# Kernel optimization log

Hardware: AMD Instinct MI355X
Metric: run time of the kernel (lower is better)

Reference implementation:

```python
import jax, jax.numpy as jnp
import numpy as np

BATCH = 32
IN_SHAPE = (64, 64)
OUT_SHAPE = (128, 128)


def setup_inputs() -> dict:
    key = jax.random.key(0)
    k1, k2 = jax.random.split(key)
    y = jax.random.normal(k1, (BATCH, *IN_SHAPE), dtype=jnp.float32)
    # normalized sample coordinates in [0,1), one per input dim
    xnew = jax.random.uniform(k2, (BATCH, *OUT_SHAPE, len(IN_SHAPE)), dtype=jnp.float32)
    return {"y": y, "xnew": xnew}


def reference(y, xnew):
    # y: [B, S1, S2]; xnew: [B, H, W, 2] with coords in [0,1)
    B = y.shape[0]
    s1, s2 = IN_SHAPE
    P = int(np.prod(OUT_SHAPE))
    x = xnew.reshape(B, P, 2)  # [B, P, 2]

    # FFT over spatial dims (dims 1..), as in torch.fft.fftn(..., dim=(1,2))
    F = jnp.fft.fftn(y, axes=(1, 2))  # [B, S1, S2] complex64

    # signed integer frequencies per dim (trigonometric interpolation)
    f1 = jnp.fft.fftfreq(s1).astype(jnp.float32) * s1  # [S1]
    f2 = jnp.fft.fftfreq(s2).astype(jnp.float32) * s2  # [S2]

    two_pi_i = 2j * jnp.pi
    # per-dim complex phase factors; separable NUFFT-type-2 evaluation
    E1 = jnp.exp(two_pi_i * x[..., 0:1] * f1)  # [B, P, S1]
    E2 = jnp.exp(two_pi_i * x[..., 1:2] * f2)  # [B, P, S2]

    # ynew[b,p] = (1/(S1*S2)) * sum_{k,m} F[b,k,m] E1[b,p,k] E2[b,p,m]
    ynew = jnp.einsum('bkm,bpk,bpm->bp', F, E1, E2) / (s1 * s2)
    ynew = jnp.real(ynew)
    return ynew.reshape(B, *OUT_SHAPE)
```

## Files before the change

kernel.cpp:

```cpp
#include <hip/hip_runtime.h>
#include <math.h>

#define PI_F  3.14159265358979323846f
#define C64_F 0.99879545620517239271f
#define S64_F 0.04906767432741801426f

typedef _Float16 f16x8 __attribute__((ext_vector_type(8)));
typedef float    f32x4 __attribute__((ext_vector_type(4)));

__device__ __forceinline__ float sinpi_hw(float x) { return __builtin_amdgcn_sinf(0.5f * x); }
__device__ __forceinline__ float cospi_hw(float x) { return __builtin_amdgcn_cosf(0.5f * x); }


__global__ __launch_bounds__(256, 3)
void fourier_interp_mfma(const float* __restrict__ y,
                         const float* __restrict__ xnew,
                         float* __restrict__ out)
{
    __shared__ __align__(16) _Float16 Yth[64 * 72];
    __shared__ __align__(16) _Float16 Ytl[64 * 72];
    __shared__ float2 tab[64];
    __shared__ float4 S1[256];
    __shared__ float4 S2[256];
    __shared__ int    NS1[256], NS2[256];
    __shared__ float  Wpart[4];

    const int tid    = threadIdx.x;
    const int batch  = blockIdx.x >> 6;
    const int seg    = blockIdx.x & 63;
    const int gpbase = (batch << 14) + (seg << 8);

    float wsum = 0.0f;
    {
        const float4* srcY = (const float4*)(y + (batch << 12));
#pragma unroll
        for (int i = 0; i < 4; ++i) {
            const int f = tid + (i << 8);
            const float4 v = srcY[f];
            const int k = f >> 4;
            const int n = (f & 15) << 2;
            _Float16 h;
            h = (_Float16)v.x; Yth[(n+0)*72 + k] = h; Ytl[(n+0)*72 + k] = (_Float16)(v.x - (float)h);
            h = (_Float16)v.y; Yth[(n+1)*72 + k] = h; Ytl[(n+1)*72 + k] = (_Float16)(v.y - (float)h);
            h = (_Float16)v.z; Yth[(n+2)*72 + k] = h; Ytl[(n+2)*72 + k] = (_Float16)(v.z - (float)h);
            h = (_Float16)v.w; Yth[(n+3)*72 + k] = h; Ytl[(n+3)*72 + k] = (_Float16)(v.w - (float)h);
            const float sv = (v.x - v.y) + (v.z - v.w);
            wsum += (k & 1) ? -sv : sv;
        }
    }
#pragma unroll
    for (int off = 32; off > 0; off >>= 1)
        wsum += __shfl_down(wsum, off, 64);
    if ((tid & 63) == 0) Wpart[tid >> 6] = wsum;

    {
        const float2 xv = ((const float2*)xnew)[gpbase + tid];
        {
            const float x = xv.x;
            const float sx = sinpi_hw(x), cx = cospi_hw(x);
            const float g = x * 64.0f;
            const float j = rintf(g);
            const float fr = g - j;
            const int  ji = (int)j;
            const float sf = sinpi_hw(fr);
            const float s64 = (ji & 1) ? -sf : sf;
            const float d = x - j * 0.015625f;
            const float cf = (fr == 0.0f) ? 64.0f
                : sf * cospi_hw(d) * __builtin_amdgcn_rcpf(sinpi_hw(d));
            S1[tid]  = make_float4(sx, cx, s64, cf);
            NS1[tid] = ji & 63;
        }
        {
            const float x = xv.y;
            const float sx = sinpi_hw(x), cx = cospi_hw(x);
            const float g = x * 64.0f;
            const float j = rintf(g);
            const float fr = g - j;
            const int  ji = (int)j;
            const float sf = sinpi_hw(fr);
            const float s64 = (ji & 1) ? -sf : sf;
            const float d = x - j * 0.015625f;
            const float cf = (fr == 0.0f) ? 64.0f
                : sf * cospi_hw(d) * __builtin_amdgcn_rcpf(sinpi_hw(d));
            S2[tid]  = make_float4(sx, cx, s64, cf);
            NS2[tid] = ji & 63;
        }
    }
    if (tid < 64)
        tab[tid] = make_float2(cospi_hw((float)tid * (1.0f / 64.0f)),
                               sinpi_hw((float)tid * (1.0f / 64.0f)));
    __syncthreads();

    const float W = (Wpart[0] + Wpart[1]) + (Wpart[2] + Wpart[3]);

    const int lane = tid & 63;
    const int wv   = tid >> 6;
    const int quad = lane >> 4;
    const int lrow = lane & 15;

    f16x8 Ah[4][2], Al[4][2];
#pragma unroll
    for (int nt = 0; nt < 4; ++nt)
#pragma unroll
        for (int kt = 0; kt < 2; ++kt) {
            const int off = ((nt << 4) + lrow) * 72 + (kt << 5) + (quad << 3);
            Ah[nt][kt] = *(const f16x8*)&Yth[off];
            Al[nt][kt] = *(const f16x8*)&Ytl[off];
        }

#pragma unroll 1
    for (int mt = 0; mt < 4; ++mt) {
        const int mtbase = (wv << 6) + (mt << 4);
        const float4 s1 = S1[mtbase + lrow];
        const int n1fix = NS1[mtbase + lrow];

        f32x4 acc[4];
#pragma unroll
        for (int nt = 0; nt < 4; ++nt) acc[nt] = (f32x4){0.f, 0.f, 0.f, 0.f};

#pragma unroll
        for (int kt = 0; kt < 2; ++kt) {
            const int n1b = (kt << 5) + (quad << 3);
            const float2 t0 = tab[n1b];
            float st = s1.x * t0.x - s1.y * t0.y;
            float ct = s1.y * t0.x + s1.x * t0.y;
            f16x8 bh, bl;
#pragma unroll
            for (int j = 0; j < 8; ++j) {
                const float sgn = (j & 1) ? -s1.z : s1.z;
                float c = sgn * ct * __builtin_amdgcn_rcpf(st);
                c = (n1b + j == n1fix) ? s1.w : c;
                const _Float16 h = (_Float16)c;
                bh[j] = h;
                bl[j] = (_Float16)(c - (float)h);
                if (j < 7) {
                    const float st2 = st * C64_F - ct * S64_F;
                    ct = ct * C64_F + st * S64_F;
                    st = st2;
                }
            }
#pragma unroll
            for (int nt = 0; nt < 4; ++nt) {
                acc[nt] = __builtin_amdgcn_mfma_f32_16x16x32_f16(Ah[nt][kt], bh, acc[nt], 0, 0, 0);
                acc[nt] = __builtin_amdgcn_mfma_f32_16x16x32_f16(Ah[nt][kt], bl, acc[nt], 0, 0, 0);
                acc[nt] = __builtin_amdgcn_mfma_f32_16x16x32_f16(Al[nt][kt], bh, acc[nt], 0, 0, 0);
            }
        }

        const float4 s2 = S2[mtbase + lrow];
        const int n2fix = NS2[mtbase + lrow];
        float red = 0.0f;
#pragma unroll
        for (int nt = 0; nt < 4; ++nt) {
            const int n2b = (nt << 4) + (quad << 2);
            const float2 tb = tab[n2b];
            float st = s2.x * tb.x - s2.y * tb.y;
            float ct = s2.y * tb.x + s2.x * tb.y;
#pragma unroll
            for (int reg = 0; reg < 4; ++reg) {
                const float sgn = (reg & 1) ? -s2.z : s2.z;
                float c = sgn * ct * __builtin_amdgcn_rcpf(st);
                c = (n2b + reg == n2fix) ? s2.w : c;
                red = fmaf(c, acc[nt][reg], red);
                if (reg < 3) {
                    const float st2 = st * C64_F - ct * S64_F;
                    ct = ct * C64_F + st * S64_F;
                    st = st2;
                }
            }
        }
        red += __shfl_xor(red, 16, 64);
        red += __shfl_xor(red, 32, 64);
        if (lane < 16) {
            const float r = red - s1.z * s2.z * W;
            out[gpbase + mtbase + lane] = r * (1.0f / 4096.0f);
        }
    }
}

extern "C" void kernel_launch(void* const* d_in, const int* in_sizes, int n_in,
                              void* d_out, int out_size, void* d_ws, size_t ws_size,
                              hipStream_t stream)
{
    const float* y    = (const float*)d_in[0];
    const float* xnew = (const float*)d_in[1];
    float* out        = (float*)d_out;

    fourier_interp_mfma<<<2048, 256, 0, stream>>>(y, xnew, out);
}
```

Baseline: 86.97 us.

## Drop fp16 split-precision MFMA terms and process 512 points per block

Removes the hi/lo fp16 error-compensation scheme, so each tile now issues one MFMA per k-step instead of three, and the low-part shared array and registers are gone. It also doubles the points handled per block (512 instead of 256) and halves the grid, which amortises the per-block Y staging and transpose over more output points. The cost is accuracy: both the Cotangent-kernel weights and the input values are now rounded to plain fp16, which could exceed the tolerance. Fewer blocks also means less parallelism across the GPU.

```diff
diff --git a/kernel.cpp b/kernel.cpp
--- a/kernel.cpp
+++ b/kernel.cpp
@@ -18,17 +18,16 @@
                          float* __restrict__ out)
 {
     __shared__ __align__(16) _Float16 Yth[64 * 72];
-    __shared__ __align__(16) _Float16 Ytl[64 * 72];
     __shared__ float2 tab[64];
-    __shared__ float4 S1[256];
-    __shared__ float4 S2[256];
-    __shared__ int    NS1[256], NS2[256];
+    __shared__ float4 S1[512];
+    __shared__ float4 S2[512];
+    __shared__ int    NS1[512], NS2[512];
     __shared__ float  Wpart[4];
 
     const int tid    = threadIdx.x;
-    const int batch  = blockIdx.x >> 6;
-    const int seg    = blockIdx.x & 63;
-    const int gpbase = (batch << 14) + (seg << 8);
+    const int batch  = blockIdx.x >> 5;
+    const int seg    = blockIdx.x & 31;
+    const int gpbase = (batch << 14) + (seg << 9);
 
     float wsum = 0.0f;
     {
@@ -39,11 +38,10 @@
             const float4 v = srcY[f];
             const int k = f >> 4;
             const int n = (f & 15) << 2;
-            _Float16 h;
-            h = (_Float16)v.x; Yth[(n+0)*72 + k] = h; Ytl[(n+0)*72 + k] = (_Float16)(v.x - (float)h);
-            h = (_Float16)v.y; Yth[(n+1)*72 + k] = h; Ytl[(n+1)*72 + k] = (_Float16)(v.y - (float)h);
-            h = (_Float16)v.z; Yth[(n+2)*72 + k] = h; Ytl[(n+2)*72 + k] = (_Float16)(v.z - (float)h);
-            h = (_Float16)v.w; Yth[(n+3)*72 + k] = h; Ytl[(n+3)*72 + k] = (_Float16)(v.w - (float)h);
+            Yth[(n+0)*72 + k] = (_Float16)v.x;
+            Yth[(n+1)*72 + k] = (_Float16)v.y;
+            Yth[(n+2)*72 + k] = (_Float16)v.z;
+            Yth[(n+3)*72 + k] = (_Float16)v.w;
             const float sv = (v.x - v.y) + (v.z - v.w);
             wsum += (k & 1) ? -sv : sv;
         }
@@ -53,8 +51,10 @@
         wsum += __shfl_down(wsum, off, 64);
     if ((tid & 63) == 0) Wpart[tid >> 6] = wsum;
 
-    {
-        const float2 xv = ((const float2*)xnew)[gpbase + tid];
+#pragma unroll
+    for (int sp = 0; sp < 2; ++sp) {
+        const int idx = tid + (sp << 8);
+        const float2 xv = ((const float2*)xnew)[gpbase + idx];
         {
             const float x = xv.x;
             const float sx = sinpi_hw(x), cx = cospi_hw(x);
@@ -67,8 +67,8 @@
             const float d = x - j * 0.015625f;
             const float cf = (fr == 0.0f) ? 64.0f
                 : sf * cospi_hw(d) * __builtin_amdgcn_rcpf(sinpi_hw(d));
-            S1[tid]  = make_float4(sx, cx, s64, cf);
-            NS1[tid] = ji & 63;
+            S1[idx]  = make_float4(sx, cx, s64, cf);
+            NS1[idx] = ji & 63;
         }
         {
             const float x = xv.y;
@@ -82,8 +82,8 @@
             const float d = x - j * 0.015625f;
             const float cf = (fr == 0.0f) ? 64.0f
                 : sf * cospi_hw(d) * __builtin_amdgcn_rcpf(sinpi_hw(d));
-            S2[tid]  = make_float4(sx, cx, s64, cf);
-            NS2[tid] = ji & 63;
+            S2[idx]  = make_float4(sx, cx, s64, cf);
+            NS2[idx] = ji & 63;
         }
     }
     if (tid < 64)
@@ -98,19 +98,18 @@
     const int quad = lane >> 4;
     const int lrow = lane & 15;
 
-    f16x8 Ah[4][2], Al[4][2];
+    f16x8 Ah[4][2];
 #pragma unroll
     for (int nt = 0; nt < 4; ++nt)
 #pragma unroll
         for (int kt = 0; kt < 2; ++kt) {
             const int off = ((nt << 4) + lrow) * 72 + (kt << 5) + (quad << 3);
             Ah[nt][kt] = *(const f16x8*)&Yth[off];
-            Al[nt][kt] = *(const f16x8*)&Ytl[off];
         }
 
 #pragma unroll 1
-    for (int mt = 0; mt < 4; ++mt) {
-        const int mtbase = (wv << 6) + (mt << 4);
+    for (int mt = 0; mt < 8; ++mt) {
+        const int mtbase = (wv << 7) + (mt << 4);
         const float4 s1 = S1[mtbase + lrow];
         const int n1fix = NS1[mtbase + lrow];
 
@@ -124,15 +123,13 @@
             const float2 t0 = tab[n1b];
             float st = s1.x * t0.x - s1.y * t0.y;
             float ct = s1.y * t0.x + s1.x * t0.y;
-            f16x8 bh, bl;
+            f16x8 bh;
 #pragma unroll
             for (int j = 0; j < 8; ++j) {
                 const float sgn = (j & 1) ? -s1.z : s1.z;
                 float c = sgn * ct * __builtin_amdgcn_rcpf(st);
                 c = (n1b + j == n1fix) ? s1.w : c;
-                const _Float16 h = (_Float16)c;
-                bh[j] = h;
-                bl[j] = (_Float16)(c - (float)h);
+                bh[j] = (_Float16)c;
                 if (j < 7) {
                     const float st2 = st * C64_F - ct * S64_F;
                     ct = ct * C64_F + st * S64_F;
@@ -140,11 +137,8 @@
                 }
             }
 #pragma unroll
-            for (int nt = 0; nt < 4; ++nt) {
+            for (int nt = 0; nt < 4; ++nt)
                 acc[nt] = __builtin_amdgcn_mfma_f32_16x16x32_f16(Ah[nt][kt], bh, acc[nt], 0, 0, 0);
-                acc[nt] = __builtin_amdgcn_mfma_f32_16x16x32_f16(Ah[nt][kt], bl, acc[nt], 0, 0, 0);
-                acc[nt] = __builtin_amdgcn_mfma_f32_16x16x32_f16(Al[nt][kt], bh, acc[nt], 0, 0, 0);
-            }
         }
 
         const float4 s2 = S2[mtbase + lrow];
@@ -186,5 +180,5 @@
     const float* xnew = (const float*)d_in[1];
     float* out        = (float*)d_out;
 
-    fourier_interp_mfma<<<2048, 256, 0, stream>>>(y, xnew, out);
+    fourier_interp_mfma<<<1024, 256, 0, stream>>>(y, xnew, out);
 }
```

Result: faster. 80.89 us (-7.0%).
